# Kernel optimization log

Measured on AMD Instinct MI355X. Metric: run time of the kernel, lower is better.

The kernel has to match this reference:

```python
import jax, jax.numpy as jnp
import numpy as np

N, T, D, H = 128, 128, 1024, 1024


def setup_inputs() -> dict:
    key = jax.random.key(0)
    k_x, k_A, k_wx, k_wh, k_wa = jax.random.split(key, 5)
    x = jax.random.normal(k_x, (N, T, D), dtype=jnp.float32)
    A = jax.random.normal(k_A, (N, H, 4, 4), dtype=jnp.float32)
    Wx = jax.random.normal(k_wx, (D, 4 * H), dtype=jnp.float32) / np.sqrt(D)
    Wh = jax.random.normal(k_wh, (H, 4 * H), dtype=jnp.float32) / np.sqrt(H)
    Wattn = jax.random.normal(k_wa, (H, 4 * H), dtype=jnp.float32) / np.sqrt(H)
    b = jnp.zeros((4 * H,), dtype=jnp.float32)
    return {"x": x, "A": A, "Wx": Wx, "Wh": Wh, "Wattn": Wattn, "b": b}


def reference(x, A, Wx, Wh, Wattn, b):
    n, h_dim = A.shape[0], A.shape[1]
    A_flat = A.reshape(n, h_dim, 16)          # (N, H, 16) spatial flattened
    h0 = A_flat.mean(axis=-1)                 # meanpool over 4x4 grid
    c0 = h0
    scale = 1.0 / np.sqrt(h_dim).astype(np.float32)

    def step(carry, x_t):
        h, c = carry
        # scaled dot-product attention over 16 spatial cells
        attn_w = jax.nn.softmax(jnp.einsum('nh,nhk->nk', h, A_flat) * scale, axis=-1)
        attn = jnp.einsum('nhk,nk->nh', A_flat, attn_w)
        a = x_t @ Wx + h @ Wh + attn @ Wattn + b   # (N, 4H)
        a_i, a_f, a_o, a_g = jnp.split(a, 4, axis=1)
        c_next = jax.nn.sigmoid(a_f) * c + jax.nn.sigmoid(a_i) * jnp.tanh(a_g)
        h_next = jax.nn.sigmoid(a_o) * jnp.tanh(c_next)
        return (h_next, c_next), h_next

    xs = jnp.transpose(x, (1, 0, 2))          # (T, N, D)
    _, hs = jax.lax.scan(step, (h0, c0), xs)  # hs: (T, N, H)
    return jnp.transpose(hs, (1, 0, 2))       # (N, T, H)
```

## Files before the change

kernel.cpp:

```cpp
#include <hip/hip_runtime.h>
#include <math.h>

#define NB 128
#define TT 128
#define HD 1024
#define FH 4096
#define QB 16
#define QSLOT (QB * 2048)

typedef __attribute__((ext_vector_type(8))) short short8v;
typedef __attribute__((ext_vector_type(4))) float float4v;

__device__ __forceinline__ ushort f2b(float f) {
    union { float f; unsigned u; } v; v.f = f;
    unsigned r = (v.u + 0x7fffu + ((v.u >> 16) & 1u)) >> 16;
    return (ushort)r;
}
__device__ __forceinline__ float b2f(ushort u) {
    union { unsigned u; float f; } v; v.u = ((unsigned)u) << 16;
    return v.f;
}
__device__ __forceinline__ float sigm(float x) { return 1.f / (1.f + __expf(-x)); }
__device__ __forceinline__ void gll16(const void* g, void* l) {
    __builtin_amdgcn_global_load_lds(
        (const __attribute__((address_space(1))) void*)g,
        (__attribute__((address_space(3))) void*)l,
        16, 0, 0);
}
__device__ __forceinline__ int swz(int c, int r) {
    return (c & 8) | ((c & 7) ^ (r & 7));
}

__global__ __launch_bounds__(256) void cvt_x(const float* __restrict__ x,
                                             ushort* __restrict__ xb) {
    size_t i = (size_t)blockIdx.x * 256 + threadIdx.x;
    const float4* p = (const float4*)x + i * 2;
    float4 va = p[0], vb = p[1];
    union { ushort u[8]; uint4 v; } o;
    o.u[0] = f2b(va.x); o.u[1] = f2b(va.y); o.u[2] = f2b(va.z); o.u[3] = f2b(va.w);
    o.u[4] = f2b(vb.x); o.u[5] = f2b(vb.y); o.u[6] = f2b(vb.z); o.u[7] = f2b(vb.w);
    ((uint4*)xb)[i] = o.v;
}

__global__ __launch_bounds__(256) void build_wt(const float* __restrict__ Wx,
                                                const float* __restrict__ Wh,
                                                const float* __restrict__ Wattn,
                                                ushort* __restrict__ WT) {
    __shared__ ushort Ls[64][65];
    int k0 = blockIdx.x * 64, n0 = blockIdx.y * 64;
    const float* W; int m;
    if (k0 < 1024)      { W = Wx;    m = 0; }
    else if (k0 < 2048) { W = Wh;    m = 1; }
    else                { W = Wattn; m = 2; }
    const int kk0 = k0 - m * 1024;
    ushort* dstm = WT + (size_t)m * FH * 1024;
    int t = threadIdx.x;
    int cc = t & 63, r4 = t >> 6;
#pragma unroll
    for (int i = 0; i < 16; ++i) {
        int r = i * 4 + r4;
        Ls[r][cc] = f2b(W[(size_t)(kk0 + r) * FH + n0 + cc]);
    }
    __syncthreads();
#pragma unroll
    for (int i = 0; i < 16; ++i) {
        int nn = i * 4 + r4;
        dstm[(size_t)(n0 + nn) * 1024 + kk0 + cc] = Ls[cc][nn];
    }
}

__global__ __launch_bounds__(256) void init_kernel(
    const float* __restrict__ Aflat, float* __restrict__ cbuf,
    ushort* __restrict__ h0buf, ushort* __restrict__ Ab16,
    float* __restrict__ qk0, float* __restrict__ qk1)
{
    __shared__ float red[4][16];
    const int n = blockIdx.x, tid = threadIdx.x;
    const int wv = tid >> 6, l = tid & 63;
    float p[16];
#pragma unroll
    for (int k = 0; k < 16; ++k) p[k] = 0.f;
#pragma unroll
    for (int u = 0; u < 4; ++u) {
        const int h = tid + u * 256;
        const size_t idx = (size_t)n * 1024 + h;
        const float4* a4 = (const float4*)(Aflat + idx * 16);
        float ar[16];
#pragma unroll
        for (int q = 0; q < 4; ++q) {
            float4 v = a4[q];
            ar[q*4+0]=v.x; ar[q*4+1]=v.y; ar[q*4+2]=v.z; ar[q*4+3]=v.w;
        }
        union { ushort us[16]; uint4 v[2]; } ob;
#pragma unroll
        for (int k = 0; k < 16; ++k) ob.us[k] = f2b(ar[k]);
        uint4* dst = (uint4*)(Ab16 + idx * 16);
        dst[0] = ob.v[0]; dst[1] = ob.v[1];

        float s = 0.f;
#pragma unroll
        for (int k = 0; k < 16; ++k) s += ar[k];
        float hv = s * 0.0625f;
        cbuf[idx] = hv;
        h0buf[idx] = f2b(hv);
#pragma unroll
        for (int k = 0; k < 16; ++k) p[k] += hv * ar[k];
    }
#pragma unroll
    for (int k = 0; k < 16; ++k) {
        float v = p[k];
        v += __shfl_xor(v, 32); v += __shfl_xor(v, 16); v += __shfl_xor(v, 8);
        v += __shfl_xor(v, 4);  v += __shfl_xor(v, 2);  v += __shfl_xor(v, 1);
        p[k] = v;
    }
    if (l == 0) {
#pragma unroll
        for (int k = 0; k < 16; ++k) red[wv][k] = p[k];
    }
    __syncthreads();
    if (tid < 16) {
        float val = red[0][tid] + red[1][tid] + red[2][tid] + red[3][tid];
#pragma unroll
        for (int bkt = 0; bkt < QB; ++bkt) {
            qk0[bkt * 2048 + n * 16 + tid] = (bkt == 0) ? val : 0.f;
            qk1[bkt * 2048 + n * 16 + tid] = 0.f;
        }
    }
}

__global__ __launch_bounds__(256) void p_gemm(
    const ushort* __restrict__ Ab16,
    const ushort* __restrict__ WatT,
    ushort* __restrict__ P2)
{
    __shared__ ushort ALDS[4 * 16 * 72];
    __shared__ ushort Bs[256 * 64];
    const int tid = threadIdx.x;
    const int wv = tid >> 6, l = tid & 63;
    const int lr = l & 15, g = l >> 4;
    const int jt = blockIdx.x, n0 = blockIdx.y * 4;
    const int snn = tid >> 6, shl = tid & 63;

    float4v acc[4][4];
#pragma unroll
    for (int i = 0; i < 4; ++i)
#pragma unroll
        for (int j = 0; j < 4; ++j) acc[i][j] = (float4v){0.f, 0.f, 0.f, 0.f};

#pragma unroll 1
    for (int kc = 0; kc < 16; ++kc) {
        __syncthreads();
        {
            const ushort* src = Ab16 + ((size_t)(n0 + snn) * 1024 + kc * 64 + shl) * 16;
            union { uint4 v[2]; ushort us[16]; } iv;
            iv.v[0] = *(const uint4*)src;
            iv.v[1] = *(const uint4*)(src + 8);
#pragma unroll
            for (int k = 0; k < 16; ++k)
                ALDS[(snn * 16 + k) * 72 + shl] = iv.us[k];
        }
#pragma unroll
        for (int i = 0; i < 8; ++i) {
            int s = i * 256 + tid;
            int r = s >> 3, c = (s & 7) ^ (r & 7);
            gll16(WatT + (size_t)(jt * 256 + r) * 1024 + kc * 64 + c * 8,
                  &Bs[s * 8]);
        }
        __syncthreads();
#pragma unroll
        for (int sub = 0; sub < 2; ++sub) {
            short8v af[4], bf[4];
#pragma unroll
            for (int nn = 0; nn < 4; ++nn)
                af[nn] = *(const short8v*)&ALDS[(nn * 16 + lr) * 72 + sub * 32 + g * 8];
#pragma unroll
            for (int nf = 0; nf < 4; ++nf) {
                int rb = wv * 64 + nf * 16 + lr;
                bf[nf] = *(const short8v*)&Bs[rb * 64 + (((sub * 4 + g) ^ (rb & 7)) * 8)];
            }
#pragma unroll
            for (int nn = 0; nn < 4; ++nn)
#pragma unroll
                for (int nf = 0; nf < 4; ++nf)
                    acc[nn][nf] = __builtin_amdgcn_mfma_f32_16x16x32_bf16(
                        af[nn], bf[nf], acc[nn][nf], 0, 0, 0);
        }
    }

#pragma unroll
    for (int nn = 0; nn < 4; ++nn)
#pragma unroll
        for (int nf = 0; nf < 4; ++nf) {
            const int j = jt * 256 + wv * 64 + nf * 16 + lr;
            union { ushort u[4]; uint2 v; } o;
#pragma unroll
            for (int jj = 0; jj < 4; ++jj) o.u[jj] = f2b(acc[nn][nf][jj]);
            *(uint2*)&P2[((size_t)(n0 + nn) * FH + j) * 16 + g * 4] = o.v;
        }
}

__global__ __launch_bounds__(256) void xa_gemm2(
    const float* __restrict__ x,
    const ushort* __restrict__ WxT,
    ushort* __restrict__ xab)
{
    __shared__ ushort As[2][128 * 64];
    __shared__ ushort Bs[2][128 * 64];
    const int tid = threadIdx.x;
    const int w = tid >> 6, l = tid & 63;
    const int wm = w >> 1, wn = w & 1;
    const int lr = l & 15, g = l >> 4;
    const int n0 = blockIdx.x * 128;
    const int mt = blockIdx.y;
    const float* Ax = x + (size_t)mt * 128 * 1024;
    const ushort* Bb = WxT + (size_t)n0 * 1024;

#define STAGEA(b, kf)                                                          \
    do {                                                                       \
        _Pragma("unroll")                                                      \
        for (int i = 0; i < 4; ++i) {                                          \
            int u = i * 256 + tid;                                             \
            int r = u >> 3, c = u & 7;                                         \
            const float* s = Ax + (size_t)r * 1024 + (kf) + c * 8;             \
            float4 v0 = *(const float4*)s;                                     \
            float4 v1 = *(const float4*)(s + 4);                               \
            union { ushort us[8]; uint4 v; } o;                                \
            o.us[0]=f2b(v0.x); o.us[1]=f2b(v0.y); o.us[2]=f2b(v0.z);           \
            o.us[3]=f2b(v0.w); o.us[4]=f2b(v1.x); o.us[5]=f2b(v1.y);           \
            o.us[6]=f2b(v1.z); o.us[7]=f2b(v1.w);                              \
            *(uint4*)&As[b][(r * 8 + (c ^ (r & 7))) * 8] = o.v;                \
        }                                                                      \
    } while (0)
#define STAGEB(b, kf)                                                          \
    do {                                                                       \
        _Pragma("unroll")                                                      \
        for (int i = 0; i < 4; ++i) {                                          \
            int s = i * 256 + tid;                                             \
            int r = s >> 3, c = s & 7;                                         \
            gll16(Bb + (size_t)r * 1024 + (kf) + (c ^ (r & 7)) * 8,            \
                  &Bs[b][s * 8]);                                              \
        }                                                                      \
    } while (0)

    float4v acc[4][4];
#pragma unroll
    for (int i = 0; i < 4; ++i)
#pragma unroll
        for (int j = 0; j < 4; ++j) acc[i][j] = (float4v){0.f, 0.f, 0.f, 0.f};

    STAGEA(0, 0);
    STAGEB(0, 0);
    __syncthreads();
    int buf = 0;
#pragma unroll 1
    for (int kc = 0; kc < 16; ++kc) {
        if (kc < 15) { STAGEA(buf ^ 1, (kc + 1) * 64); STAGEB(buf ^ 1, (kc + 1) * 64); }
        const ushort* Ab = As[buf];
        const ushort* Bbuf = Bs[buf];
#pragma unroll
        for (int sub = 0; sub < 2; ++sub) {
            short8v af[4], bf[4];
#pragma unroll
            for (int mf = 0; mf < 4; ++mf) {
                int ra = wm * 64 + mf * 16 + lr;
                af[mf] = *(const short8v*)&Ab[ra * 64 + (((sub * 4 + g) ^ (ra & 7)) * 8)];
            }
#pragma unroll
            for (int nf = 0; nf < 4; ++nf) {
                int rb = wn * 64 + nf * 16 + lr;
                bf[nf] = *(const short8v*)&Bbuf[rb * 64 + (((sub * 4 + g) ^ (rb & 7)) * 8)];
            }
#pragma unroll
            for (int mf = 0; mf < 4; ++mf)
#pragma unroll
                for (int nf = 0; nf < 4; ++nf)
                    acc[mf][nf] = __builtin_amdgcn_mfma_f32_16x16x32_bf16(
                        af[mf], bf[nf], acc[mf][nf], 0, 0, 0);
        }
        __syncthreads();
        buf ^= 1;
    }
#undef STAGEA
#undef STAGEB

#pragma unroll
    for (int mf = 0; mf < 4; ++mf)
#pragma unroll
        for (int nf = 0; nf < 4; ++nf) {
            const int col = n0 + wn * 64 + nf * 16 + lr;
#pragma unroll
            for (int j = 0; j < 4; ++j) {
                const int rl = wm * 64 + mf * 16 + g * 4 + j;
                xab[((size_t)rl * NB + mt) * FH + col] = f2b(acc[mf][nf][j]);
            }
        }
}

template <int XAF>
__global__ __launch_bounds__(256) void step_kernel(
    const ushort* __restrict__ hcur,
    ushort* __restrict__ hnext,
    const ushort* __restrict__ xb_t,
    const ushort* __restrict__ xab_t,
    const ushort* __restrict__ WxT,
    const ushort* __restrict__ WhT,
    const ushort* __restrict__ P2,
    const ushort* __restrict__ Ab16,
    const float* __restrict__ bias,
    float* __restrict__ cbuf,
    const float* __restrict__ qk_cur,
    float* __restrict__ qk_next,
    float* __restrict__ qk_zero,
    float* __restrict__ out_t)
{
    __shared__ ushort AS[16384];
    __shared__ ushort BS[16384];
    __shared__ float accL[2 * 32 * 33];
    __shared__ float wLDS[32 * 16];

    const int tid = threadIdx.x;
    const int w = tid >> 6, l = tid & 63;
    const int mh = w & 1, kh = w >> 1;
    const int lr = l & 15, g = l >> 4;

    const int bid = blockIdx.x;
    const int xcd = bid & 7, ii = bid >> 3;
    const int bx = xcd * 16 + (ii & 15);
    const int my = ii >> 4;
    const int n0 = my * 32;

    if (bid < 128) qk_zero[bid * 256 + tid] = 0.f;

    if (tid < 32) {
        const float* q = qk_cur + (n0 + tid) * 16;
        float4 s4[4];
#pragma unroll
        for (int q4 = 0; q4 < 4; ++q4) s4[q4] = ((const float4*)q)[q4];
#pragma unroll
        for (int bkt = 1; bkt < QB; ++bkt) {
            const float4* qb = (const float4*)(q + bkt * 2048);
#pragma unroll
            for (int q4 = 0; q4 < 4; ++q4) {
                float4 v = qb[q4];
                s4[q4].x += v.x; s4[q4].y += v.y; s4[q4].z += v.z; s4[q4].w += v.w;
            }
        }
        float s[16];
#pragma unroll
        for (int q4 = 0; q4 < 4; ++q4) {
            s[q4*4+0] = s4[q4].x; s[q4*4+1] = s4[q4].y;
            s[q4*4+2] = s4[q4].z; s[q4*4+3] = s4[q4].w;
        }
        float m = -1e30f;
#pragma unroll
        for (int k = 0; k < 16; ++k) { s[k] *= 0.03125f; m = fmaxf(m, s[k]); }
        float sum = 0.f;
#pragma unroll
        for (int k = 0; k < 16; ++k) { s[k] = __expf(s[k] - m); sum += s[k]; }
        float inv = 1.f / sum;
#pragma unroll
        for (int k = 0; k < 16; ++k) wLDS[tid * 16 + k] = s[k] * inv;
    }

#define STAGE(b, kc)                                                           \
    do {                                                                       \
        _Pragma("unroll")                                                      \
        for (int i = 0; i < 4; ++i) {                                          \
            int u = i * 256 + tid;                                             \
            int skh = u >> 9, rem = u & 511;                                   \
            int r = rem >> 4, c = rem & 15;                                    \
            int lc = swz(c, r);                                                \
            const ushort* src;                                                 \
            if (XAF == 1)                                                      \
                src = hcur + (size_t)(n0 + r) * 1024 + skh * 512               \
                      + (kc) * 128 + lc * 8;                                   \
            else                                                               \
                src = skh                                                      \
                    ? hcur + (size_t)(n0 + r) * 1024 + (kc) * 128 + lc * 8     \
                    : xb_t + (size_t)(n0 + r) * (TT * HD) + (kc) * 128 + lc * 8;\
            gll16(src, AS + (((b) * 2 + skh) * 512 + rem) * 8);                \
        }                                                                      \
        _Pragma("unroll")                                                      \
        for (int i = 0; i < 4; ++i) {                                          \
            int u = i * 256 + tid;                                             \
            int skh = u >> 9, rem = u & 511;                                   \
            int r = rem >> 4, c = rem & 15;                                    \
            int lc = swz(c, r);                                                \
            int jg = (r >> 3) * 1024 + bx * 8 + (r & 7);                       \
            const ushort* src;                                                 \
            if (XAF == 1)                                                      \
                src = WhT + (size_t)jg * 1024 + skh * 512 + (kc) * 128 + lc * 8;\
            else                                                               \
                src = (skh ? WhT : WxT) + (size_t)jg * 1024                    \
                      + (kc) * 128 + lc * 8;                                   \
            gll16(src, BS + (((b) * 2 + skh) * 512 + rem) * 8);                \
        }                                                                      \
    } while (0)

    float4v acc[2];
    acc[0] = (float4v){0.f, 0.f, 0.f, 0.f};
    acc[1] = (float4v){0.f, 0.f, 0.f, 0.f};

    const int NK = (XAF == 1) ? 4 : 8;
    STAGE(0, 0);
    __syncthreads();
    int buf = 0;
#pragma unroll 1
    for (int kc = 0; kc < NK; ++kc) {
        if (kc + 1 < NK) STAGE(buf ^ 1, kc + 1);
        const int base = (buf * 2 + kh) * 512;
        const int ra = mh * 16 + lr;
#pragma unroll
        for (int ks = 0; ks < 4; ++ks) {
            const int c = ks * 4 + g;
            short8v af = *(const short8v*)&AS[(base + ra * 16 + swz(c, ra)) * 8];
#pragma unroll
            for (int nf = 0; nf < 2; ++nf) {
                const int rb = nf * 16 + lr;
                short8v bf = *(const short8v*)&BS[(base + rb * 16 + swz(c, rb)) * 8];
                acc[nf] = __builtin_amdgcn_mfma_f32_16x16x32_bf16(af, bf, acc[nf], 0, 0, 0);
            }
        }
        __syncthreads();
        buf ^= 1;
    }
#undef STAGE

#pragma unroll
    for (int nf = 0; nf < 2; ++nf)
#pragma unroll
        for (int jj = 0; jj < 4; ++jj)
            accL[(kh * 32 + mh * 16 + g * 4 + jj) * 33 + nf * 16 + lr] = acc[nf][jj];
    __syncthreads();

    const int n_l = tid >> 3, hcl = tid & 7;
    const int n = n0 + n_l;
    const int hc = bx * 8 + hcl;

    float wv_[16];
#pragma unroll
    for (int k = 0; k < 16; ++k) wv_[k] = wLDS[n_l * 16 + k];

    float val[4];
#pragma unroll
    for (int q = 0; q < 4; ++q) {
        const int cq = q * 8 + hcl;
        float v = accL[n_l * 33 + cq] + accL[(32 + n_l) * 33 + cq]
                + bias[q * 1024 + hc];
        if (XAF == 1) v += b2f(xab_t[(size_t)n * FH + q * 1024 + hc]);
        const ushort* pp = P2 + ((size_t)n * FH + q * 1024 + hc) * 16;
        union { uint4 v[2]; ushort us[16]; } pv;
        pv.v[0] = *(const uint4*)pp;
        pv.v[1] = *(const uint4*)(pp + 8);
#pragma unroll
        for (int k = 0; k < 16; ++k) v += wv_[k] * b2f(pv.us[k]);
        val[q] = v;
    }

    const size_t chidx = (size_t)n * 1024 + hc;
    float cn = sigm(val[1]) * cbuf[chidx] + sigm(val[0]) * tanhf(val[3]);
    float hv = sigm(val[2]) * tanhf(cn);
    cbuf[chidx] = cn;
    out_t[(size_t)n * (TT * HD) + hc] = hv;
    hnext[chidx] = f2b(hv);

    union { uint4 v[2]; ushort us[16]; } av;
    {
        const ushort* ap = Ab16 + chidx * 16;
        av.v[0] = *(const uint4*)ap;
        av.v[1] = *(const uint4*)(ap + 8);
    }
    float vv[16];
#pragma unroll
    for (int k = 0; k < 16; ++k) vv[k] = hv * b2f(av.us[k]);
    {
        bool hi = (hcl & 1);
#pragma unroll
        for (int q = 0; q < 8; ++q) {
            float send = hi ? vv[q] : vv[q + 8];
            float recv = __shfl_xor(send, 1);
            vv[q] = (hi ? vv[q + 8] : vv[q]) + recv;
        }
        hi = (hcl & 2);
#pragma unroll
        for (int q = 0; q < 4; ++q) {
            float send = hi ? vv[q] : vv[q + 4];
            float recv = __shfl_xor(send, 2);
            vv[q] = (hi ? vv[q + 4] : vv[q]) + recv;
        }
        hi = (hcl & 4);
#pragma unroll
        for (int q = 0; q < 2; ++q) {
            float send = hi ? vv[q] : vv[q + 2];
            float recv = __shfl_xor(send, 4);
            vv[q] = (hi ? vv[q + 2] : vv[q]) + recv;
        }
    }
    const int kbase = ((hcl & 1) << 3) | ((hcl & 2) << 1) | ((hcl & 4) >> 1);
    float* qdst = qk_next + (bx & (QB - 1)) * 2048 + n * 16;
    atomicAdd(qdst + kbase,     vv[0]);
    atomicAdd(qdst + kbase + 1, vv[1]);
}

extern "C" void kernel_launch(void* const* d_in, const int* in_sizes, int n_in,
                              void* d_out, int out_size, void* d_ws, size_t ws_size,
                              hipStream_t stream) {
    const float* x     = (const float*)d_in[0];
    const float* A     = (const float*)d_in[1];
    const float* Wx    = (const float*)d_in[2];
    const float* Wh    = (const float*)d_in[3];
    const float* Wattn = (const float*)d_in[4];
    const float* b     = (const float*)d_in[5];
    float* out = (float*)d_out;

    ushort* WT   = (ushort*)d_ws;
    ushort* WxT  = WT;
    ushort* WhT  = WT + (size_t)FH * 1024;
    ushort* WatT = WT + (size_t)2 * FH * 1024;
    ushort* Ab16 = WT + (size_t)3 * FH * 1024;
    ushort* hb   = Ab16 + (size_t)NB * HD * 16;
    float*  cb   = (float*)(hb + (size_t)2 * NB * HD);
    float*  qk   = cb + (size_t)NB * HD;
    ushort* P2   = (ushort*)(qk + 3 * QSLOT);
    ushort* tail = P2 + (size_t)NB * FH * 16;

    const size_t base  = (size_t)((char*)tail - (char*)d_ws);
    const size_t xasz  = (size_t)TT * NB * FH * 2;
    const size_t xbsz  = (size_t)NB * TT * HD * 2;

    build_wt<<<dim3(48, 64), 256, 0, stream>>>(Wx, Wh, Wattn, WT);
    init_kernel<<<NB, 256, 0, stream>>>(A, cb, hb, Ab16, qk, qk + QSLOT);
    p_gemm<<<dim3(16, 32), 256, 0, stream>>>(Ab16, WatT, P2);

    if (ws_size >= base + xasz) {
        ushort* xab = tail;
        xa_gemm2<<<dim3(32, 128), 256, 0, stream>>>(x, WxT, xab);
        for (int t = 0; t < TT; ++t) {
            const ushort* hc = hb + (size_t)(t & 1) * NB * HD;
            ushort* hn       = hb + (size_t)((t + 1) & 1) * NB * HD;
            const float* qc  = qk + (size_t)(t % 3) * QSLOT;
            float* qn        = qk + (size_t)((t + 1) % 3) * QSLOT;
            float* qz        = qk + (size_t)((t + 2) % 3) * QSLOT;
            step_kernel<1><<<512, 256, 0, stream>>>(
                hc, hn, nullptr, xab + (size_t)t * NB * FH, WxT, WhT, P2, Ab16,
                b, cb, qc, qn, qz, out + (size_t)t * HD);
        }
    } else {
        ushort* xb = tail;
        cvt_x<<<8192, 256, 0, stream>>>(x, xb);
        for (int t = 0; t < TT; ++t) {
            const ushort* hc = hb + (size_t)(t & 1) * NB * HD;
            ushort* hn       = hb + (size_t)((t + 1) & 1) * NB * HD;
            const float* qc  = qk + (size_t)(t % 3) * QSLOT;
            float* qn        = qk + (size_t)((t + 1) % 3) * QSLOT;
            float* qz        = qk + (size_t)((t + 2) % 3) * QSLOT;
            step_kernel<0><<<512, 256, 0, stream>>>(
                hc, hn, xb + (size_t)t * HD, nullptr, WxT, WhT, P2, Ab16,
                b, cb, qc, qn, qz, out + (size_t)t * HD);
        }
    }
}
```

Baseline: 1.737 ms.

## Pre-convert x to bf16, remap xa GEMM blocks by XCD, hoist staging and fast tanh

When enough workspace exists, x is converted to bf16 once and the input-projection GEMM then loads its A tiles through direct global-to-LDS loads instead of converting fp32 in registers. The GEMM grid is flattened and remapped so blocks sharing the same row tile land on the same XCD for L2 reuse. In the step kernel, the first tile staging is issued before the softmax-weight computation so the loads overlap it. tanhf and the divisions are replaced with rcp/exp-based approximations. The cost is an extra conversion pass, extra workspace, and slightly lower transcendental accuracy.

```diff
diff --git a/kernel.cpp b/kernel.cpp
--- a/kernel.cpp
+++ b/kernel.cpp
@@ -20,7 +20,12 @@
     union { unsigned u; float f; } v; v.u = ((unsigned)u) << 16;
     return v.f;
 }
-__device__ __forceinline__ float sigm(float x) { return 1.f / (1.f + __expf(-x)); }
+__device__ __forceinline__ float sigm(float x) {
+    return __builtin_amdgcn_rcpf(1.f + __expf(-x));
+}
+__device__ __forceinline__ float tanh_fast(float x) {
+    return 1.f - 2.f * __builtin_amdgcn_rcpf(1.f + __expf(2.f * x));
+}
 __device__ __forceinline__ void gll16(const void* g, void* l) {
     __builtin_amdgcn_global_load_lds(
         (const __attribute__((address_space(1))) void*)g,
@@ -199,8 +204,10 @@
         }
 }
 
-__global__ __launch_bounds__(256) void xa_gemm2(
+template <int B16A>
+__global__ __launch_bounds__(256) void xa_gemm3(
     const float* __restrict__ x,
+    const ushort* __restrict__ xb,
     const ushort* __restrict__ WxT,
     ushort* __restrict__ xab)
 {
@@ -210,32 +217,47 @@
     const int w = tid >> 6, l = tid & 63;
     const int wm = w >> 1, wn = w & 1;
     const int lr = l & 15, g = l >> 4;
-    const int n0 = blockIdx.x * 128;
-    const int mt = blockIdx.y;
-    const float* Ax = x + (size_t)mt * 128 * 1024;
-    const ushort* Bb = WxT + (size_t)n0 * 1024;
+
+    const int bid = blockIdx.x;
+    const int xcd = bid & 7, ii = bid >> 3;
+    const int mt = xcd * 16 + (ii & 15);
+    const int n0 = (ii >> 4) * 128;
+
+    const float*  Ax  = x  + (size_t)mt * 128 * 1024;
+    const ushort* Axb = xb + (size_t)mt * 128 * 1024;
+    const ushort* Bb  = WxT + (size_t)n0 * 1024;
 
 #define STAGEA(b, kf)                                                          \
     do {                                                                       \
-        _Pragma("unroll")                                                      \
-        for (int i = 0; i < 4; ++i) {                                          \
-            int u = i * 256 + tid;                                             \
-            int r = u >> 3, c = u & 7;                                         \
-            const float* s = Ax + (size_t)r * 1024 + (kf) + c * 8;             \
-            float4 v0 = *(const float4*)s;                                     \
-            float4 v1 = *(const float4*)(s + 4);                               \
-            union { ushort us[8]; uint4 v; } o;                                \
-            o.us[0]=f2b(v0.x); o.us[1]=f2b(v0.y); o.us[2]=f2b(v0.z);           \
-            o.us[3]=f2b(v0.w); o.us[4]=f2b(v1.x); o.us[5]=f2b(v1.y);           \
-            o.us[6]=f2b(v1.z); o.us[7]=f2b(v1.w);                              \
-            *(uint4*)&As[b][(r * 8 + (c ^ (r & 7))) * 8] = o.v;                \
+        if (B16A) {                                                            \
+            _Pragma("unroll")                                                  \
+            for (int i = 0; i < 4; ++i) {                                      \
+                int s = i * 256 + tid;                                         \
+                int r = s >> 3, c = s & 7;                                     \
+                gll16(Axb + (size_t)r * 1024 + (kf) + (c ^ (r & 7)) * 8,       \
+                      &As[b][s * 8]);                                          \
+            }                                                                  \
+        } else {                                                               \
+            _Pragma("unroll")                                                  \
+            for (int i = 0; i < 4; ++i) {                                      \
+                int u = i * 256 + tid;                                         \
+                int r = u >> 3, c = u & 7;                                     \
+                const float* s = Ax + (size_t)r * 1024 + (kf) + c * 8;         \
+                float4 v0 = *(const float4*)s;                                 \
+                float4 v1 = *(const float4*)(s + 4);                           \
+                union { ushort us[8]; uint4 v; } o;                            \
+                o.us[0]=f2b(v0.x); o.us[1]=f2b(v0.y); o.us[2]=f2b(v0.z);       \
+                o.us[3]=f2b(v0.w); o.us[4]=f2b(v1.x); o.us[5]=f2b(v1.y);       \
+                o.us[6]=f2b(v1.z); o.us[7]=f2b(v1.w);                          \
+                *(uint4*)&As[b][(r * 8 + (c ^ (r & 7))) * 8] = o.v;            \
+            }                                                                  \
         }                                                                      \
     } while (0)
 #define STAGEB(b, kf)                                                          \
     do {                                                                       \
         _Pragma("unroll")                                                      \
-        for (int i = 0; i < 4; ++i) {                                          \
-            int s = i * 256 + tid;                                             \
+        for (int s2 = 0; s2 < 4; ++s2) {                                       \
+            int s = s2 * 256 + tid;                                            \
             int r = s >> 3, c = s & 7;                                         \
             gll16(Bb + (size_t)r * 1024 + (kf) + (c ^ (r & 7)) * 8,            \
                   &Bs[b][s * 8]);                                              \
@@ -328,39 +350,6 @@
     const int bx = xcd * 16 + (ii & 15);
     const int my = ii >> 4;
     const int n0 = my * 32;
-
-    if (bid < 128) qk_zero[bid * 256 + tid] = 0.f;
-
-    if (tid < 32) {
-        const float* q = qk_cur + (n0 + tid) * 16;
-        float4 s4[4];
-#pragma unroll
-        for (int q4 = 0; q4 < 4; ++q4) s4[q4] = ((const float4*)q)[q4];
-#pragma unroll
-        for (int bkt = 1; bkt < QB; ++bkt) {
-            const float4* qb = (const float4*)(q + bkt * 2048);
-#pragma unroll
-            for (int q4 = 0; q4 < 4; ++q4) {
-                float4 v = qb[q4];
-                s4[q4].x += v.x; s4[q4].y += v.y; s4[q4].z += v.z; s4[q4].w += v.w;
-            }
-        }
-        float s[16];
-#pragma unroll
-        for (int q4 = 0; q4 < 4; ++q4) {
-            s[q4*4+0] = s4[q4].x; s[q4*4+1] = s4[q4].y;
-            s[q4*4+2] = s4[q4].z; s[q4*4+3] = s4[q4].w;
-        }
-        float m = -1e30f;
-#pragma unroll
-        for (int k = 0; k < 16; ++k) { s[k] *= 0.03125f; m = fmaxf(m, s[k]); }
-        float sum = 0.f;
-#pragma unroll
-        for (int k = 0; k < 16; ++k) { s[k] = __expf(s[k] - m); sum += s[k]; }
-        float inv = 1.f / sum;
-#pragma unroll
-        for (int k = 0; k < 16; ++k) wLDS[tid * 16 + k] = s[k] * inv;
-    }
 
 #define STAGE(b, kc)                                                           \
     do {                                                                       \
@@ -397,12 +386,46 @@
         }                                                                      \
     } while (0)
 
+    STAGE(0, 0);
+
+    if (bid < 128) qk_zero[bid * 256 + tid] = 0.f;
+
+    if (tid < 32) {
+        const float* q = qk_cur + (n0 + tid) * 16;
+        float4 s4[4];
+#pragma unroll
+        for (int q4 = 0; q4 < 4; ++q4) s4[q4] = ((const float4*)q)[q4];
+#pragma unroll
+        for (int bkt = 1; bkt < QB; ++bkt) {
+            const float4* qb = (const float4*)(q + bkt * 2048);
+#pragma unroll
+            for (int q4 = 0; q4 < 4; ++q4) {
+                float4 v = qb[q4];
+                s4[q4].x += v.x; s4[q4].y += v.y; s4[q4].z += v.z; s4[q4].w += v.w;
+            }
+        }
+        float s[16];
+#pragma unroll
+        for (int q4 = 0; q4 < 4; ++q4) {
+            s[q4*4+0] = s4[q4].x; s[q4*4+1] = s4[q4].y;
+            s[q4*4+2] = s4[q4].z; s[q4*4+3] = s4[q4].w;
+        }
+        float m = -1e30f;
+#pragma unroll
+        for (int k = 0; k < 16; ++k) { s[k] *= 0.03125f; m = fmaxf(m, s[k]); }
+        float sum = 0.f;
+#pragma unroll
+        for (int k = 0; k < 16; ++k) { s[k] = __expf(s[k] - m); sum += s[k]; }
+        float inv = __builtin_amdgcn_rcpf(sum);
+#pragma unroll
+        for (int k = 0; k < 16; ++k) wLDS[tid * 16 + k] = s[k] * inv;
+    }
+
     float4v acc[2];
     acc[0] = (float4v){0.f, 0.f, 0.f, 0.f};
     acc[1] = (float4v){0.f, 0.f, 0.f, 0.f};
 
     const int NK = (XAF == 1) ? 4 : 8;
-    STAGE(0, 0);
     __syncthreads();
     int buf = 0;
 #pragma unroll 1
@@ -458,8 +481,8 @@
     }
 
     const size_t chidx = (size_t)n * 1024 + hc;
-    float cn = sigm(val[1]) * cbuf[chidx] + sigm(val[0]) * tanhf(val[3]);
-    float hv = sigm(val[2]) * tanhf(cn);
+    float cn = sigm(val[1]) * cbuf[chidx] + sigm(val[0]) * tanh_fast(val[3]);
+    float hv = sigm(val[2]) * tanh_fast(cn);
     cbuf[chidx] = cn;
     out_t[(size_t)n * (TT * HD) + hc] = hv;
     hnext[chidx] = f2b(hv);
@@ -534,7 +557,13 @@
 
     if (ws_size >= base + xasz) {
         ushort* xab = tail;
-        xa_gemm2<<<dim3(32, 128), 256, 0, stream>>>(x, WxT, xab);
+        if (ws_size >= base + xasz + xbsz) {
+            ushort* xb = tail + xasz / 2;
+            cvt_x<<<8192, 256, 0, stream>>>(x, xb);
+            xa_gemm3<1><<<4096, 256, 0, stream>>>(nullptr, xb, WxT, xab);
+        } else {
+            xa_gemm3<0><<<4096, 256, 0, stream>>>(x, nullptr, WxT, xab);
+        }
         for (int t = 0; t < TT; ++t) {
             const ushort* hc = hb + (size_t)(t & 1) * NB * HD;
             ushort* hn       = hb + (size_t)((t + 1) & 1) * NB * HD;
```

Result: faster. 1.674 ms (-3.6%).
